# Performance work log

Hardware: AMD Instinct MI355X
Metric: run time of the kernel (lower is better)

Reference implementation:

```python
import jax, jax.numpy as jnp
import numpy as np

M = 512  # mem_dim

def silu(x):
    return x * jax.nn.sigmoid(x)

def layernorm(x, g, b, eps=1e-5):
    m = jnp.mean(x, axis=-1, keepdims=True)
    v = jnp.mean((x - m) ** 2, axis=-1, keepdims=True)
    return (x - m) * jax.lax.rsqrt(v + eps) * g + b

def dwconv(x, w, b):
    # x: [B,S,C], w: [C,1,K] depthwise, same padding
    y = jax.lax.conv_general_dilated(
        x.transpose(0, 2, 1), w, (1,), [(1, 1)],
        dimension_numbers=('NCH', 'OIH', 'NCH'), feature_group_count=x.shape[-1])
    return (y + b[None, :, None]).transpose(0, 2, 1)

def mlp(p, inp):
    W1, b1, W2, b2 = p
    return silu(inp @ W1.T + b1) @ W2.T + b2

def coeff(x, W1, b1, W2, b2):
    # x: [B,S,D] -> sigmoid scalar per token, averaged over batch -> [S]
    h = silu(jnp.einsum('bsd,hd->bsh', x, W1) + b1)
    c = jax.nn.sigmoid(jnp.einsum('bsh,oh->bso', h, W2) + b2)[..., 0]
    return jnp.mean(c, axis=0)

def setup_inputs() -> dict:
    key = jax.random.key(0)
    ks = jax.random.split(key, 24)
    B, S, D, H, CH, K = 8, 1024, 512, 32, 16, 3
    g = lambda k, shape, fan: jax.random.normal(k, shape, jnp.float32) / np.sqrt(fan)
    return {
        'x': jax.random.normal(ks[0], (B, S, D), jnp.float32),
        'Wk': g(ks[1], (M, D), D), 'Wv': g(ks[2], (M, D), D), 'Wq': g(ks[3], (M, D), D),
        'ck_w': g(ks[4], (M, 1, K), K), 'ck_b': g(ks[5], (M,), K),
        'cv_w': g(ks[6], (M, 1, K), K), 'cv_b': g(ks[7], (M,), K),
        'cq_w': g(ks[8], (M, 1, K), K), 'cq_b': g(ks[9], (M,), K),
        'ln_g': jnp.ones((M,), jnp.float32), 'ln_b': jnp.zeros((M,), jnp.float32),
        'W1': g(ks[10], (H, M), M), 'b1': jnp.zeros((H,), jnp.float32),
        'W2': g(ks[11], (M, H), H), 'b2': jnp.zeros((M,), jnp.float32),
        'aW1': g(ks[12], (CH, D), D), 'ab1': jnp.zeros((CH,), jnp.float32),
        'aW2': g(ks[13], (1, CH), CH), 'ab2': -2.0 * jnp.ones((1,), jnp.float32),
        'tW1': g(ks[14], (CH, D), D), 'tb1': jnp.zeros((CH,), jnp.float32),
        'tW2': g(ks[15], (1, CH), CH), 'tb2': -2.0 * jnp.ones((1,), jnp.float32),
        'eW1': g(ks[16], (CH, D), D), 'eb1': jnp.zeros((CH,), jnp.float32),
        'eW2': g(ks[17], (1, CH), CH), 'eb2': -2.0 * jnp.ones((1,), jnp.float32),
    }

def reference(x, Wk, Wv, Wq, ck_w, ck_b, cv_w, cv_b, cq_w, cq_b, ln_g, ln_b,
              W1, b1, W2, b2, aW1, ab1, aW2, ab2, tW1, tb1, tW2, tb2,
              eW1, eb1, eW2, eb2):
    k = layernorm(dwconv(x @ Wk.T, ck_w, ck_b), ln_g, ln_b)
    v = dwconv(x @ Wv.T, cv_w, cv_b)
    q = layernorm(dwconv(x @ Wq.T, cq_w, cq_b), ln_g, ln_b)
    alpha = coeff(x, aW1, ab1, aW2, ab2)  # [S]
    theta = coeff(x, tW1, tb1, tW2, tb2)
    eta = coeff(x, eW1, eb1, eW2, eb2)

    params0 = (W1, b1, W2, b2)
    S0 = jax.tree_util.tree_map(jnp.zeros_like, params0)

    def step(carry, xs_t):
        p, Sm = carry
        kt, vt, qt, a, th, e = xs_t  # kt/vt/qt: [B,M], a/th/e: scalar
        y = mlp(p, qt)  # output with pre-update params
        grad = jax.grad(lambda pp: jnp.mean((mlp(pp, kt) - vt) ** 2))(p)
        Sm = jax.tree_util.tree_map(lambda s, gi: e * s - th * gi, Sm, grad)
        p = jax.tree_util.tree_map(lambda pi, si: (1.0 - a) * pi + si, p, Sm)
        return (p, Sm), y

    xs = (k.transpose(1, 0, 2), v.transpose(1, 0, 2), q.transpose(1, 0, 2),
          alpha, theta, eta)
    _, ys = jax.lax.scan(step, (params0, S0), xs)
    return ys.transpose(1, 0, 2)  # [B,S,M]
```

## Files before the change

### kernel.cpp

```cpp
#include <hip/hip_runtime.h>
#include <hip/hip_bf16.h>
#include <cstdint>
#include <cstddef>

typedef __attribute__((ext_vector_type(8))) short bf16x8;
typedef __attribute__((ext_vector_type(4))) float f32x4;

#define DEV static __device__ __forceinline__

DEV float bf2f(uint16_t u){ union{uint32_t i; float f;} c; c.i = ((uint32_t)u) << 16; return c.f; }
DEV uint16_t f2bf(float f){ union{float f; uint32_t i;} c; c.f = f; uint32_t r = c.i + 0x7FFFu + ((c.i >> 16) & 1u); return (uint16_t)(r >> 16); }

DEV f32x4 mfma16(bf16x8 a, bf16x8 b, f32x4 c){
  return __builtin_amdgcn_mfma_f32_16x16x32_bf16(a, b, c, 0, 0, 0);
}

__global__ __launch_bounds__(128) void nltm_coeff(
    const float* __restrict__ x,
    const float* __restrict__ aW1, const float* __restrict__ ab1,
    const float* __restrict__ aW2, const float* __restrict__ ab2,
    const float* __restrict__ tW1, const float* __restrict__ tb1,
    const float* __restrict__ tW2, const float* __restrict__ tb2,
    const float* __restrict__ eW1, const float* __restrict__ eb1,
    const float* __restrict__ eW2, const float* __restrict__ eb2,
    float* __restrict__ gates)
{
  const int s = blockIdx.x, z = blockIdx.y;
  const int b = threadIdx.x >> 4, ch = threadIdx.x & 15;
  const float* w1 = (z==0)?aW1:(z==1)?tW1:eW1;
  const float* c1 = (z==0)?ab1:(z==1)?tb1:eb1;
  const float* w2 = (z==0)?aW2:(z==1)?tW2:eW2;
  const float* c2 = (z==0)?ab2:(z==1)?tb2:eb2;
  const float4* xp = (const float4*)(x + ((size_t)(b << 10) + s)*512);
  const float4* wp = (const float4*)(w1 + ch*512);
  float dot = 0.f;
  #pragma unroll 4
  for (int i = 0; i < 128; ++i){
    float4 a = xp[i], c = wp[i];
    dot += a.x*c.x + a.y*c.y + a.z*c.z + a.w*c.w;
  }
  dot += c1[ch];
  const float sg = 1.f / (1.f + __expf(-dot));
  float v = dot * sg * w2[ch];
  v += __shfl_xor(v, 1, 64);
  v += __shfl_xor(v, 2, 64);
  v += __shfl_xor(v, 4, 64);
  v += __shfl_xor(v, 8, 64);
  if (ch == 0){
    const float cc = 1.f / (1.f + __expf(-(v + c2[0])));
    atomicAdd(gates + (z << 10) + s, cc * 0.125f);
  }
}

__global__ __launch_bounds__(256) void nltm_gemm(
    const float* __restrict__ x, const float* __restrict__ Wk,
    const float* __restrict__ Wv, const float* __restrict__ Wq,
    uint16_t* __restrict__ preK, uint16_t* __restrict__ preV, uint16_t* __restrict__ preQ)
{
  __shared__ float As[16][132];
  __shared__ float Bs[16][132];
  const float* W = (blockIdx.z == 0) ? Wk : (blockIdx.z == 1) ? Wv : Wq;
  uint16_t* op  = (blockIdx.z == 0) ? preK : (blockIdx.z == 1) ? preV : preQ;
  const int tid = threadIdx.x;
  const int n0 = blockIdx.x << 7, m0 = blockIdx.y << 7;
  const int r = tid >> 1, cs = (tid & 1) << 3;
  const int ty = tid >> 4, tx = tid & 15;
  float acc[8][8];
  #pragma unroll
  for (int i = 0; i < 8; ++i)
    #pragma unroll
    for (int j = 0; j < 8; ++j) acc[i][j] = 0.f;

  for (int k0 = 0; k0 < 512; k0 += 16){
    float4 a0 = *(const float4*)(x + (size_t)(n0 + r)*512 + k0 + cs);
    float4 a1 = *(const float4*)(x + (size_t)(n0 + r)*512 + k0 + cs + 4);
    float4 b0 = *(const float4*)(W + (size_t)(m0 + r)*512 + k0 + cs);
    float4 b1 = *(const float4*)(W + (size_t)(m0 + r)*512 + k0 + cs + 4);
    __syncthreads();
    As[cs+0][r]=a0.x; As[cs+1][r]=a0.y; As[cs+2][r]=a0.z; As[cs+3][r]=a0.w;
    As[cs+4][r]=a1.x; As[cs+5][r]=a1.y; As[cs+6][r]=a1.z; As[cs+7][r]=a1.w;
    Bs[cs+0][r]=b0.x; Bs[cs+1][r]=b0.y; Bs[cs+2][r]=b0.z; Bs[cs+3][r]=b0.w;
    Bs[cs+4][r]=b1.x; Bs[cs+5][r]=b1.y; Bs[cs+6][r]=b1.z; Bs[cs+7][r]=b1.w;
    __syncthreads();
    #pragma unroll
    for (int kk = 0; kk < 16; ++kk){
      float4 av0 = *(const float4*)&As[kk][ty*8];
      float4 av1 = *(const float4*)&As[kk][ty*8+4];
      float4 bv0 = *(const float4*)&Bs[kk][tx*8];
      float4 bv1 = *(const float4*)&Bs[kk][tx*8+4];
      const float aa[8] = {av0.x,av0.y,av0.z,av0.w,av1.x,av1.y,av1.z,av1.w};
      const float bb[8] = {bv0.x,bv0.y,bv0.z,bv0.w,bv1.x,bv1.y,bv1.z,bv1.w};
      #pragma unroll
      for (int i = 0; i < 8; ++i)
        #pragma unroll
        for (int j = 0; j < 8; ++j)
          acc[i][j] = fmaf(aa[i], bb[j], acc[i][j]);
    }
  }
  #pragma unroll
  for (int i = 0; i < 8; ++i){
    const size_t n = (size_t)(n0 + ty*8 + i);
    uint4 v;
    v.x = (uint32_t)f2bf(acc[i][0]) | ((uint32_t)f2bf(acc[i][1]) << 16);
    v.y = (uint32_t)f2bf(acc[i][2]) | ((uint32_t)f2bf(acc[i][3]) << 16);
    v.z = (uint32_t)f2bf(acc[i][4]) | ((uint32_t)f2bf(acc[i][5]) << 16);
    v.w = (uint32_t)f2bf(acc[i][6]) | ((uint32_t)f2bf(acc[i][7]) << 16);
    *(uint4*)(op + n*512 + m0 + tx*8) = v;
  }
}

__global__ __launch_bounds__(512) void nltm_conv(
    const uint16_t* __restrict__ preK, const uint16_t* __restrict__ preV, const uint16_t* __restrict__ preQ,
    const float* __restrict__ ckw, const float* __restrict__ ckb,
    const float* __restrict__ cvw, const float* __restrict__ cvb,
    const float* __restrict__ cqw, const float* __restrict__ cqb,
    const float* __restrict__ lng, const float* __restrict__ lnb,
    uint16_t* __restrict__ postK, uint16_t* __restrict__ postV, uint16_t* __restrict__ postQ)
{
  const int z = blockIdx.y;
  const int b = blockIdx.x >> 10, s = blockIdx.x & 1023;
  const int m = threadIdx.x;
  const uint16_t* pre = (z==0)?preK:(z==1)?preV:preQ;
  const float* w  = (z==0)?ckw:(z==1)?cvw:cqw;
  const float* wb = (z==0)?ckb:(z==1)?cvb:cqb;
  uint16_t* post = (z==0)?postK:(z==1)?postV:postQ;
  const size_t base = ((size_t)(b << 10) + s)*512 + m;
  const float xm = (s > 0)    ? bf2f(pre[base - 512]) : 0.f;
  const float x0 = bf2f(pre[base]);
  const float xp = (s < 1023) ? bf2f(pre[base + 512]) : 0.f;
  float y = fmaf(w[m*3], xm, fmaf(w[m*3+1], x0, fmaf(w[m*3+2], xp, wb[m])));
  if (z != 1){
    __shared__ float red[2][8];
    float s1 = y, s2 = y*y;
    #pragma unroll
    for (int o = 32; o > 0; o >>= 1){
      s1 += __shfl_xor(s1, o, 64);
      s2 += __shfl_xor(s2, o, 64);
    }
    if ((threadIdx.x & 63) == 0){ red[0][threadIdx.x>>6] = s1; red[1][threadIdx.x>>6] = s2; }
    __syncthreads();
    float t1 = 0.f, t2 = 0.f;
    #pragma unroll
    for (int i = 0; i < 8; ++i){ t1 += red[0][i]; t2 += red[1][i]; }
    const float mean = t1 * (1.f/512.f);
    const float var  = t2 * (1.f/512.f) - mean*mean;
    y = (y - mean) * rsqrtf(var + 1e-5f) * lng[m] + lnb[m];
  }
  post[((size_t)(s << 3) + b)*512 + m] = f2bf(y);
}

__global__ __launch_bounds__(512, 2) void nltm_scan(
    const float* __restrict__ W1g, const float* __restrict__ b1g,
    const float* __restrict__ W2g, const float* __restrict__ b2g,
    const float* __restrict__ gates,
    const uint16_t* __restrict__ kq, const uint16_t* __restrict__ vq,
    const uint16_t* __restrict__ qq, float* __restrict__ out)
{
  constexpr uint32_t W1Lo=0, W2Lo=33280, W2To=66048, QLo=99328, KLo=107520,
                     VTo=115712, KTo=123904, GOTo=132096, HQSo=140288, HKSo=140928,
                     HKSTo=141568, GSITo=142080, GPTo=142592, SCRo=143104,
                     B1o=151296, B2o=151424;
  __shared__ __align__(16) char smem[153472];
  const int tid = threadIdx.x;
  const int lane = tid & 63;
  const int wid = tid >> 6;
  const int rb = lane & 15;
  const int kg = lane >> 4;

  float* b1L = (float*)(smem + B1o);
  float* b2L = (float*)(smem + B2o);

  float w1m[8][4], sm1[8][4], w2a[8][4], sma[8][4];
  #pragma unroll
  for (int i = 0; i < 8; ++i){
    const int tt = i >> 1, ht = i & 1;
    const int mA = (wid*4 + tt)*16;
    #pragma unroll
    for (int j = 0; j < 4; ++j){
      const int h1 = ht*16 + rb, m1 = mA + kg*4 + j;
      w1m[i][j] = W1g[h1*512 + m1];  sm1[i][j] = 0.f;
      w2a[i][j] = W2g[m1*32 + h1];   sma[i][j] = 0.f;
    }
  }
  float b2m = b2g[tid], smb2 = 0.f;
  float b1m = (tid < 32) ? b1g[tid] : 0.f, smb1 = 0.f;

  for (int idx = tid; idx < 16384; idx += 512){
    const int h = idx >> 9, m = idx & 511;
    *(uint16_t*)(smem + W1Lo + h*1040 + m*2) = f2bf(W1g[idx]);
    const int m2 = idx >> 5, h2 = idx & 31;
    const float w2v = W2g[idx];
    *(uint16_t*)(smem + W2Lo + m2*64 + (((h2>>3)^(m2&3))<<4) + ((h2&7)<<1)) = f2bf(w2v);
    *(uint16_t*)(smem + W2To + h2*1040 + m2*2) = f2bf(w2v);
  }
  if (tid < 32) b1L[tid] = b1g[tid];
  b2L[tid] = b2g[tid];

  #pragma unroll
  for (int i = 0; i < 4; ++i){
    const int g = ((i & 1) << 9) + tid;
    const int b = g >> 7, m4 = (g & 127) << 2;
    const uint16_t* src = (i < 2) ? kq : qq;
    uint2 v = *(const uint2*)(src + b*512 + m4);
    *(uint2*)(smem + ((i<2)?KLo:QLo) + b*1024 + (((m4>>3)^(b&7))<<4) + ((m4&7)<<1)) = v;
  }
  {
    const uint16_t* kp = kq + tid;
    const uint16_t* vp = vq + tid;
    uint32_t a0=kp[0],a1=kp[512],a2=kp[1024],a3=kp[1536],a4=kp[2048],a5=kp[2560],a6=kp[3072],a7=kp[3584];
    uint4 kt4; kt4.x=a0|(a1<<16); kt4.y=a2|(a3<<16); kt4.z=a4|(a5<<16); kt4.w=a6|(a7<<16);
    *(uint4*)(smem + KTo + tid*16) = kt4;
    uint32_t c0=vp[0],c1=vp[512],c2=vp[1024],c3=vp[1536],c4=vp[2048],c5=vp[2560],c6=vp[3072],c7=vp[3584];
    uint4 vt4; vt4.x=c0|(c1<<16); vt4.y=c2|(c3<<16); vt4.z=c4|(c5<<16); vt4.w=c6|(c7<<16);
    *(uint4*)(smem + VTo + tid*16) = vt4;
  }
  __syncthreads();

  const f32x4 cz = {0.f, 0.f, 0.f, 0.f};
  const bf16x8 zf = {0,0,0,0,0,0,0,0};

  for (int t = 0; t < 1024; ++t){
    const int tn = (t < 1023) ? (t + 1) : 1023;
    uint2 pf[4];
    #pragma unroll
    for (int i = 0; i < 4; ++i){
      const int g = ((i & 1) << 9) + tid;
      const int b = g >> 7, m4 = (g & 127) << 2;
      const uint16_t* src = (i < 2) ? kq : qq;
      pf[i] = *(const uint2*)(src + (size_t)tn*4096 + b*512 + m4);
    }
    uint4 ktpf, vtpf;
    {
      const uint16_t* kp = kq + (size_t)tn*4096 + tid;
      const uint16_t* vp = vq + (size_t)tn*4096 + tid;
      uint32_t a0=kp[0],a1=kp[512],a2=kp[1024],a3=kp[1536],a4=kp[2048],a5=kp[2560],a6=kp[3072],a7=kp[3584];
      ktpf.x=a0|(a1<<16); ktpf.y=a2|(a3<<16); ktpf.z=a4|(a5<<16); ktpf.w=a6|(a7<<16);
      uint32_t c0=vp[0],c1=vp[512],c2=vp[1024],c3=vp[1536],c4=vp[2048],c5=vp[2560],c6=vp[3072],c7=vp[3584];
      vtpf.x=c0|(c1<<16); vtpf.y=c2|(c3<<16); vtpf.z=c4|(c5<<16); vtpf.w=c6|(c7<<16);
    }
    const float a_t = gates[t], th_t = gates[1024 + t], e_t = gates[2048 + t];
    const float oma = 1.f - a_t;

    if (wid < 4){
      const int mm = wid >> 1, ht = wid & 1;
      const uint32_t srcO = mm ? KLo : QLo;
      const uint32_t w1row = W1Lo + (uint32_t)(ht*16 + rb)*1040;
      f32x4 acc0 = cz, acc1 = cz;
      #pragma unroll
      for (int k0 = 0; k0 < 16; k0 += 2){
        const int ch0 = (k0 << 2) + kg, ch1 = ((k0+1) << 2) + kg;
        bf16x8 a0 = (rb < 8) ? *(const bf16x8*)(smem + srcO + rb*1024 + ((ch0 ^ (rb&7)) << 4)) : zf;
        bf16x8 b0 = *(const bf16x8*)(smem + w1row + ((k0*32 + kg*8) << 1));
        acc0 = mfma16(a0, b0, acc0);
        bf16x8 a1 = (rb < 8) ? *(const bf16x8*)(smem + srcO + rb*1024 + ((ch1 ^ (rb&7)) << 4)) : zf;
        bf16x8 b1 = *(const bf16x8*)(smem + w1row + (((k0+1)*32 + kg*8) << 1));
        acc1 = mfma16(a1, b1, acc1);
      }
      f32x4 acc = acc0 + acc1;
      const int hh = ht*16 + rb;
      const float b1v = b1L[hh];
      float hsv[4], sdv[4];
      #pragma unroll
      for (int j = 0; j < 4; ++j){
        const float z = acc[j] + b1v;
        const float sg = 1.f / (1.f + __expf(-z));
        hsv[j] = z * sg;
        sdv[j] = sg * (1.f + z * (1.f - sg));
      }
      if (kg < 2){
        if (mm == 0){
          #pragma unroll
          for (int j = 0; j < 4; ++j)
            *(uint16_t*)(smem + HQSo + (kg*4+j)*80 + hh*2) = f2bf(hsv[j]);
        } else {
          #pragma unroll
          for (int j = 0; j < 4; ++j)
            *(uint16_t*)(smem + HKSo + (kg*4+j)*80 + hh*2) = f2bf(hsv[j]);
          uint2 hv; hv.x = (uint32_t)f2bf(hsv[0]) | ((uint32_t)f2bf(hsv[1])<<16);
                    hv.y = (uint32_t)f2bf(hsv[2]) | ((uint32_t)f2bf(hsv[3])<<16);
          *(uint2*)(smem + HKSTo + hh*16 + kg*8) = hv;
          uint2 sv; sv.x = (uint32_t)f2bf(sdv[0]) | ((uint32_t)f2bf(sdv[1])<<16);
                    sv.y = (uint32_t)f2bf(sdv[2]) | ((uint32_t)f2bf(sdv[3])<<16);
          *(uint2*)(smem + GSITo + hh*16 + kg*8) = sv;
        }
      }
    }
    __syncthreads();

    {
      bf16x8 aq = (rb < 8) ? *(const bf16x8*)(smem + HQSo + rb*80 + kg*16) : zf;
      bf16x8 ak = (rb < 8) ? *(const bf16x8*)(smem + HKSo + rb*80 + kg*16) : zf;
      #pragma unroll
      for (int i = 0; i < 4; ++i){
        const int mcol = (((wid << 2) + i) << 4) + rb;
        bf16x8 bw = *(const bf16x8*)(smem + W2Lo + mcol*64 + ((kg ^ (mcol & 3)) << 4));
        f32x4 cy = mfma16(aq, bw, cz);
        f32x4 ck = mfma16(ak, bw, cz);
        const float b2v = b2L[mcol];
        if (kg < 2){
          uint2 vvp = *(const uint2*)(smem + VTo + mcol*16 + kg*8);
          const float vv0 = bf2f((uint16_t)vvp.x), vv1 = bf2f((uint16_t)(vvp.x>>16));
          const float vv2 = bf2f((uint16_t)vvp.y), vv3 = bf2f((uint16_t)(vvp.y>>16));
          float gvv[4];
          gvv[0] = (ck[0] + b2v - vv0) * (2.f/4096.f);
          gvv[1] = (ck[1] + b2v - vv1) * (2.f/4096.f);
          gvv[2] = (ck[2] + b2v - vv2) * (2.f/4096.f);
          gvv[3] = (ck[3] + b2v - vv3) * (2.f/4096.f);
          #pragma unroll
          for (int j = 0; j < 4; ++j){
            const int bb = kg*4 + j;
            out[(((size_t)bb << 10) + t)*512 + mcol] = cy[j] + b2v;
          }
          uint2 gp; gp.x = (uint32_t)f2bf(gvv[0]) | ((uint32_t)f2bf(gvv[1])<<16);
                    gp.y = (uint32_t)f2bf(gvv[2]) | ((uint32_t)f2bf(gvv[3])<<16);
          *(uint2*)(smem + GOTo + mcol*16 + kg*8) = gp;
          #pragma unroll
          for (int j = 0; j < 4; ++j){
            const int bb = kg*4 + j;
            *(uint16_t*)(smem + KLo + bb*1024 + (((mcol>>3) ^ (bb&7))<<4) + ((mcol&7)<<1)) = f2bf(gvv[j]);
          }
        }
      }
    }
    __syncthreads();

    {
      const int ht = wid & 1, ks = wid >> 1;
      const int hcol = ht*16 + rb;
      f32x4 a0 = cz, a1 = cz;
      #pragma unroll
      for (int kk = 0; kk < 4; ++kk){
        const int mc8 = ks*16 + kk*4 + kg;
        bf16x8 av = (rb < 8) ? *(const bf16x8*)(smem + KLo + rb*1024 + ((mc8 ^ (rb&7)) << 4)) : zf;
        bf16x8 bv = *(const bf16x8*)(smem + W2To + hcol*1040 + (mc8 << 4));
        if (kk & 1) a1 = mfma16(av, bv, a1); else a0 = mfma16(av, bv, a0);
      }
      f32x4 acc = a0 + a1;
      *(f32x4*)(smem + SCRo + (((ht*4 + ks)*64 + lane) << 4)) = acc;
    }
    __syncthreads();

    if (wid < 2 && kg < 2){
      const int ht = wid;
      f32x4 s = cz;
      #pragma unroll
      for (int ks = 0; ks < 4; ++ks){
        f32x4 p = *(const f32x4*)(smem + SCRo + (((ht*4 + ks)*64 + lane) << 4));
        s += p;
      }
      uint2 gs = *(const uint2*)(smem + GSITo + (ht*16 + rb)*16 + kg*8);
      const float g0 = s[0]*bf2f((uint16_t)gs.x), g1 = s[1]*bf2f((uint16_t)(gs.x>>16));
      const float g2 = s[2]*bf2f((uint16_t)gs.y), g3 = s[3]*bf2f((uint16_t)(gs.y>>16));
      uint2 w; w.x = (uint32_t)f2bf(g0) | ((uint32_t)f2bf(g1)<<16);
               w.y = (uint32_t)f2bf(g2) | ((uint32_t)f2bf(g3)<<16);
      *(uint2*)(smem + GPTo + (ht*16 + rb)*16 + kg*8) = w;
    }
    __syncthreads();

    {
      #pragma unroll
      for (int i = 0; i < 4; ++i){
        const int g = ((i & 1) << 9) + tid;
        const int b = g >> 7, m4 = (g & 127) << 2;
        *(uint2*)(smem + ((i<2)?KLo:QLo) + b*1024 + (((m4>>3)^(b&7))<<4) + ((m4&7)<<1)) = pf[i];
      }

      bf16x8 hkF[2], gpF[2];
      #pragma unroll
      for (int ht = 0; ht < 2; ++ht){
        const int r0 = ht*16 + rb;
        hkF[ht] = (kg == 0) ? *(const bf16x8*)(smem + HKSTo + r0*16) : zf;
        gpF[ht] = (kg == 0) ? *(const bf16x8*)(smem + GPTo  + r0*16) : zf;
      }
      #pragma unroll
      for (int tt = 0; tt < 4; ++tt){
        const int mA = (wid*4 + tt)*16;
        const int r0 = mA + rb;
        bf16x8 ktf = (kg == 0) ? *(const bf16x8*)(smem + KTo  + r0*16) : zf;
        bf16x8 gof = (kg == 0) ? *(const bf16x8*)(smem + GOTo + r0*16) : zf;
        #pragma unroll
        for (int ht = 0; ht < 2; ++ht){
          const int i = tt*2 + ht;
          f32x4 g1 = mfma16(ktf, gpF[ht], cz);
          f32x4 g2 = mfma16(gof, hkF[ht], cz);
          float f1[4], f2[4];
          #pragma unroll
          for (int j = 0; j < 4; ++j){
            sm1[i][j] = e_t*sm1[i][j] - th_t*g1[j];
            w1m[i][j] = oma*w1m[i][j] + sm1[i][j];
            f1[j] = w1m[i][j];
            sma[i][j] = e_t*sma[i][j] - th_t*g2[j];
            w2a[i][j] = oma*w2a[i][j] + sma[i][j];
            f2[j] = w2a[i][j];
          }
          uint2 u1; u1.x = (uint32_t)f2bf(f1[0]) | ((uint32_t)f2bf(f1[1])<<16);
                    u1.y = (uint32_t)f2bf(f1[2]) | ((uint32_t)f2bf(f1[3])<<16);
          *(uint2*)(smem + W1Lo + (ht*16 + rb)*1040 + (mA + kg*4)*2) = u1;
          uint2 u2; u2.x = (uint32_t)f2bf(f2[0]) | ((uint32_t)f2bf(f2[1])<<16);
                    u2.y = (uint32_t)f2bf(f2[2]) | ((uint32_t)f2bf(f2[3])<<16);
          *(uint2*)(smem + W2To + (ht*16 + rb)*1040 + (mA + kg*4)*2) = u2;
        }
      }
      #pragma unroll
      for (int tt = 0; tt < 4; ++tt){
        const int m2 = (wid*4 + tt)*16 + rb;
        #pragma unroll
        for (int ht = 0; ht < 2; ++ht){
          const uint32_t cb = W2To + (uint32_t)m2*2 + (uint32_t)(ht*16 + kg*4)*1040;
          uint16_t t0 = *(const uint16_t*)(smem + cb);
          uint16_t t1 = *(const uint16_t*)(smem + cb + 1040);
          uint16_t t2 = *(const uint16_t*)(smem + cb + 2080);
          uint16_t t3 = *(const uint16_t*)(smem + cb + 3120);
          uint2 u; u.x = (uint32_t)t0 | ((uint32_t)t1<<16);
                   u.y = (uint32_t)t2 | ((uint32_t)t3<<16);
          *(uint2*)(smem + W2Lo + m2*64 + ((((ht<<1)+(kg>>1)) ^ (m2&3))<<4) + ((kg&1)<<3)) = u;
        }
      }
      {
        uint4 gv = *(const uint4*)(smem + GOTo + tid*16);
        float gb2 = bf2f((uint16_t)gv.x) + bf2f((uint16_t)(gv.x>>16))
                  + bf2f((uint16_t)gv.y) + bf2f((uint16_t)(gv.y>>16))
                  + bf2f((uint16_t)gv.z) + bf2f((uint16_t)(gv.z>>16))
                  + bf2f((uint16_t)gv.w) + bf2f((uint16_t)(gv.w>>16));
        smb2 = e_t*smb2 - th_t*gb2;
        b2m = oma*b2m + smb2;
        b2L[tid] = b2m;
      }
      if (tid < 32){
        uint4 gv = *(const uint4*)(smem + GPTo + tid*16);
        float gb1 = bf2f((uint16_t)gv.x) + bf2f((uint16_t)(gv.x>>16))
                  + bf2f((uint16_t)gv.y) + bf2f((uint16_t)(gv.y>>16))
                  + bf2f((uint16_t)gv.z) + bf2f((uint16_t)(gv.z>>16))
                  + bf2f((uint16_t)gv.w) + bf2f((uint16_t)(gv.w>>16));
        smb1 = e_t*smb1 - th_t*gb1;
        b1m = oma*b1m + smb1;
        b1L[tid] = b1m;
      }
      *(uint4*)(smem + KTo + tid*16) = ktpf;
      *(uint4*)(smem + VTo + tid*16) = vtpf;
    }
    __syncthreads();
  }
}

extern "C" void kernel_launch(void* const* d_in, const int* in_sizes, int n_in,
                              void* d_out, int out_size, void* d_ws, size_t ws_size,
                              hipStream_t stream)
{
  const float* x   = (const float*)d_in[0];
  const float* Wk  = (const float*)d_in[1];
  const float* Wv  = (const float*)d_in[2];
  const float* Wq  = (const float*)d_in[3];
  const float* ckw = (const float*)d_in[4];
  const float* ckb = (const float*)d_in[5];
  const float* cvw = (const float*)d_in[6];
  const float* cvb = (const float*)d_in[7];
  const float* cqw = (const float*)d_in[8];
  const float* cqb = (const float*)d_in[9];
  const float* lng = (const float*)d_in[10];
  const float* lnb = (const float*)d_in[11];
  const float* W1g = (const float*)d_in[12];
  const float* b1g = (const float*)d_in[13];
  const float* W2g = (const float*)d_in[14];
  const float* b2g = (const float*)d_in[15];
  const float* aW1 = (const float*)d_in[16];
  const float* ab1 = (const float*)d_in[17];
  const float* aW2 = (const float*)d_in[18];
  const float* ab2 = (const float*)d_in[19];
  const float* tW1 = (const float*)d_in[20];
  const float* tb1 = (const float*)d_in[21];
  const float* tW2 = (const float*)d_in[22];
  const float* tb2 = (const float*)d_in[23];
  const float* eW1 = (const float*)d_in[24];
  const float* eb1 = (const float*)d_in[25];
  const float* eW2 = (const float*)d_in[26];
  const float* eb2 = (const float*)d_in[27];

  char* ws = (char*)d_ws;
  float* gates = (float*)ws;
  uint16_t* preK  = (uint16_t*)(ws + 16384);
  uint16_t* preV  = preK + 4194304;
  uint16_t* preQ  = preV + 4194304;
  uint16_t* postK = preQ + 4194304;
  uint16_t* postV = postK + 4194304;
  uint16_t* postQ = postV + 4194304;

  hipMemsetAsync(gates, 0, 3*1024*sizeof(float), stream);
  nltm_coeff<<<dim3(1024,3), 128, 0, stream>>>(x, aW1,ab1,aW2,ab2, tW1,tb1,tW2,tb2,
                                               eW1,eb1,eW2,eb2, gates);
  nltm_gemm<<<dim3(64,4,3), 256, 0, stream>>>(x, Wk, Wv, Wq, preK, preV, preQ);
  nltm_conv<<<dim3(8192,3), 512, 0, stream>>>(preK,preV,preQ, ckw,ckb,cvw,cvb,cqw,cqb,
                                              lng,lnb, postK,postV,postQ);
  nltm_scan<<<dim3(1), dim3(512), 0, stream>>>(W1g, b1g, W2g, b2g, gates,
                                               postK, postV, postQ, (float*)d_out);
}
```

Before: 11.01 ms.

## Widen serial scan block to 1024 threads and pre-transpose K/V in conv

The single-block recurrent scan now runs with 1024 threads instead of 512. The first-layer MLP GEMM is split across all 16 waves with an LDS reduction, and Q and K hidden activations are stacked into one 16-row MFMA tile. The conv kernel is split into three launches and writes token-major transposed copies of K and V, so the scan loads them with vector reads instead of gathered 16-bit loads. Manual float-to-bf16 packing is replaced by v_cvt_pk_bf16_f32. In exchange, each step has an extra barrier, there is more scratch traffic through LDS, and fewer registers per thread remain under the 1024-thread launch bound.

```diff
diff --git a/kernel.cpp b/kernel.cpp
--- a/kernel.cpp
+++ b/kernel.cpp
@@ -10,6 +10,11 @@
 
 DEV float bf2f(uint16_t u){ union{uint32_t i; float f;} c; c.i = ((uint32_t)u) << 16; return c.f; }
 DEV uint16_t f2bf(float f){ union{float f; uint32_t i;} c; c.f = f; uint32_t r = c.i + 0x7FFFu + ((c.i >> 16) & 1u); return (uint16_t)(r >> 16); }
+DEV uint32_t cvtpk(float lo, float hi){
+  uint32_t r;
+  asm("v_cvt_pk_bf16_f32 %0, %1, %2" : "=v"(r) : "v"(lo), "v"(hi));
+  return r;
+}
 
 DEV f32x4 mfma16(bf16x8 a, bf16x8 b, f32x4 c){
   return __builtin_amdgcn_mfma_f32_16x16x32_bf16(a, b, c, 0, 0, 0);
@@ -110,26 +115,19 @@
 }
 
 __global__ __launch_bounds__(512) void nltm_conv(
-    const uint16_t* __restrict__ preK, const uint16_t* __restrict__ preV, const uint16_t* __restrict__ preQ,
-    const float* __restrict__ ckw, const float* __restrict__ ckb,
-    const float* __restrict__ cvw, const float* __restrict__ cvb,
-    const float* __restrict__ cqw, const float* __restrict__ cqb,
-    const float* __restrict__ lng, const float* __restrict__ lnb,
-    uint16_t* __restrict__ postK, uint16_t* __restrict__ postV, uint16_t* __restrict__ postQ)
+    const uint16_t* __restrict__ pre,
+    const float* __restrict__ w, const float* __restrict__ wb,
+    const float* __restrict__ lng, const float* __restrict__ lnb, const int doLN,
+    uint16_t* __restrict__ post, uint16_t* __restrict__ postT)
 {
-  const int z = blockIdx.y;
   const int b = blockIdx.x >> 10, s = blockIdx.x & 1023;
   const int m = threadIdx.x;
-  const uint16_t* pre = (z==0)?preK:(z==1)?preV:preQ;
-  const float* w  = (z==0)?ckw:(z==1)?cvw:cqw;
-  const float* wb = (z==0)?ckb:(z==1)?cvb:cqb;
-  uint16_t* post = (z==0)?postK:(z==1)?postV:postQ;
   const size_t base = ((size_t)(b << 10) + s)*512 + m;
   const float xm = (s > 0)    ? bf2f(pre[base - 512]) : 0.f;
   const float x0 = bf2f(pre[base]);
   const float xp = (s < 1023) ? bf2f(pre[base + 512]) : 0.f;
   float y = fmaf(w[m*3], xm, fmaf(w[m*3+1], x0, fmaf(w[m*3+2], xp, wb[m])));
-  if (z != 1){
+  if (doLN){
     __shared__ float red[2][8];
     float s1 = y, s2 = y*y;
     #pragma unroll
@@ -146,21 +144,23 @@
     const float var  = t2 * (1.f/512.f) - mean*mean;
     y = (y - mean) * rsqrtf(var + 1e-5f) * lng[m] + lnb[m];
   }
-  post[((size_t)(s << 3) + b)*512 + m] = f2bf(y);
-}
-
-__global__ __launch_bounds__(512, 2) void nltm_scan(
+  const uint16_t yb = f2bf(y);
+  if (post)  post[((size_t)(s << 3) + b)*512 + m] = yb;
+  if (postT) postT[(((size_t)s << 9) + m)*8 + b] = yb;
+}
+
+__global__ __launch_bounds__(1024) void nltm_scan(
     const float* __restrict__ W1g, const float* __restrict__ b1g,
     const float* __restrict__ W2g, const float* __restrict__ b2g,
     const float* __restrict__ gates,
-    const uint16_t* __restrict__ kq, const uint16_t* __restrict__ vq,
-    const uint16_t* __restrict__ qq, float* __restrict__ out)
+    const uint16_t* __restrict__ kN, const uint16_t* __restrict__ qN,
+    const uint16_t* __restrict__ kT, const uint16_t* __restrict__ vT,
+    float* __restrict__ out)
 {
-  constexpr uint32_t W1Lo=0, W2Lo=33280, W2To=66048, QLo=99328, KLo=107520,
-                     VTo=115712, KTo=123904, GOTo=132096, HQSo=140288, HKSo=140928,
-                     HKSTo=141568, GSITo=142080, GPTo=142592, SCRo=143104,
-                     B1o=151296, B2o=151424;
-  __shared__ __align__(16) char smem[153472];
+  constexpr uint32_t W1Lo=0, W2No=33280, W2To=66048, QKLo=99328, VTo=115712,
+                     KTo=123904, GOTo=132096, HQKo=140288, HKSTo=141312,
+                     SILPo=141824, GPTo=143872, SCRo=144384, B1o=160768, B2o=160896;
+  __shared__ __align__(16) char smem[162944];
   const int tid = threadIdx.x;
   const int lane = tid & 63;
   const int wid = tid >> 6;
@@ -170,11 +170,11 @@
   float* b1L = (float*)(smem + B1o);
   float* b2L = (float*)(smem + B2o);
 
-  float w1m[8][4], sm1[8][4], w2a[8][4], sma[8][4];
+  float w1m[4][4], sm1[4][4], w2a[4][4], sma[4][4];
   #pragma unroll
-  for (int i = 0; i < 8; ++i){
+  for (int i = 0; i < 4; ++i){
     const int tt = i >> 1, ht = i & 1;
-    const int mA = (wid*4 + tt)*16;
+    const int mA = (wid*2 + tt)*16;
     #pragma unroll
     for (int j = 0; j < 4; ++j){
       const int h1 = ht*16 + rb, m1 = mA + kg*4 + j;
@@ -182,142 +182,112 @@
       w2a[i][j] = W2g[m1*32 + h1];   sma[i][j] = 0.f;
     }
   }
-  float b2m = b2g[tid], smb2 = 0.f;
+  float b2m = (tid < 512) ? b2g[tid] : 0.f, smb2 = 0.f;
   float b1m = (tid < 32) ? b1g[tid] : 0.f, smb1 = 0.f;
 
-  for (int idx = tid; idx < 16384; idx += 512){
+  for (int idx = tid; idx < 16384; idx += 1024){
     const int h = idx >> 9, m = idx & 511;
     *(uint16_t*)(smem + W1Lo + h*1040 + m*2) = f2bf(W1g[idx]);
     const int m2 = idx >> 5, h2 = idx & 31;
     const float w2v = W2g[idx];
-    *(uint16_t*)(smem + W2Lo + m2*64 + (((h2>>3)^(m2&3))<<4) + ((h2&7)<<1)) = f2bf(w2v);
+    *(uint16_t*)(smem + W2No + m2*64 + (((h2>>3)^(m2&3))<<4) + ((h2&7)<<1)) = f2bf(w2v);
     *(uint16_t*)(smem + W2To + h2*1040 + m2*2) = f2bf(w2v);
   }
   if (tid < 32) b1L[tid] = b1g[tid];
-  b2L[tid] = b2g[tid];
-
-  #pragma unroll
-  for (int i = 0; i < 4; ++i){
-    const int g = ((i & 1) << 9) + tid;
-    const int b = g >> 7, m4 = (g & 127) << 2;
-    const uint16_t* src = (i < 2) ? kq : qq;
-    uint2 v = *(const uint2*)(src + b*512 + m4);
-    *(uint2*)(smem + ((i<2)?KLo:QLo) + b*1024 + (((m4>>3)^(b&7))<<4) + ((m4&7)<<1)) = v;
-  }
+  if (tid < 512) b2L[tid] = b2g[tid];
+
   {
-    const uint16_t* kp = kq + tid;
-    const uint16_t* vp = vq + tid;
-    uint32_t a0=kp[0],a1=kp[512],a2=kp[1024],a3=kp[1536],a4=kp[2048],a5=kp[2560],a6=kp[3072],a7=kp[3584];
-    uint4 kt4; kt4.x=a0|(a1<<16); kt4.y=a2|(a3<<16); kt4.z=a4|(a5<<16); kt4.w=a6|(a7<<16);
-    *(uint4*)(smem + KTo + tid*16) = kt4;
-    uint32_t c0=vp[0],c1=vp[512],c2=vp[1024],c3=vp[1536],c4=vp[2048],c5=vp[2560],c6=vp[3072],c7=vp[3584];
-    uint4 vt4; vt4.x=c0|(c1<<16); vt4.y=c2|(c3<<16); vt4.z=c4|(c5<<16); vt4.w=c6|(c7<<16);
-    *(uint4*)(smem + VTo + tid*16) = vt4;
+    const int b = tid >> 7, m4 = (tid & 127) << 2;
+    const uint32_t swz = (((m4>>3) ^ (b&7))<<4) + ((m4&7)<<1);
+    *(uint2*)(smem + QKLo + b*1024 + swz)       = *(const uint2*)(qN + tid*4);
+    *(uint2*)(smem + QKLo + (8+b)*1024 + swz)   = *(const uint2*)(kN + tid*4);
+    if (tid < 512) *(uint4*)(smem + KTo + tid*16) = *(const uint4*)(kT + tid*8);
+    else           *(uint4*)(smem + VTo + (tid-512)*16) = *(const uint4*)(vT + (tid-512)*8);
   }
   __syncthreads();
 
   const f32x4 cz = {0.f, 0.f, 0.f, 0.f};
   const bf16x8 zf = {0,0,0,0,0,0,0,0};
+  const int ht_ = wid & 1, ks_ = wid >> 1;
 
   for (int t = 0; t < 1024; ++t){
     const int tn = (t < 1023) ? (t + 1) : 1023;
-    uint2 pf[4];
-    #pragma unroll
-    for (int i = 0; i < 4; ++i){
-      const int g = ((i & 1) << 9) + tid;
-      const int b = g >> 7, m4 = (g & 127) << 2;
-      const uint16_t* src = (i < 2) ? kq : qq;
-      pf[i] = *(const uint2*)(src + (size_t)tn*4096 + b*512 + m4);
-    }
-    uint4 ktpf, vtpf;
-    {
-      const uint16_t* kp = kq + (size_t)tn*4096 + tid;
-      const uint16_t* vp = vq + (size_t)tn*4096 + tid;
-      uint32_t a0=kp[0],a1=kp[512],a2=kp[1024],a3=kp[1536],a4=kp[2048],a5=kp[2560],a6=kp[3072],a7=kp[3584];
-      ktpf.x=a0|(a1<<16); ktpf.y=a2|(a3<<16); ktpf.z=a4|(a5<<16); ktpf.w=a6|(a7<<16);
-      uint32_t c0=vp[0],c1=vp[512],c2=vp[1024],c3=vp[1536],c4=vp[2048],c5=vp[2560],c6=vp[3072],c7=vp[3584];
-      vtpf.x=c0|(c1<<16); vtpf.y=c2|(c3<<16); vtpf.z=c4|(c5<<16); vtpf.w=c6|(c7<<16);
-    }
+    uint2 pfq = *(const uint2*)(qN + (size_t)tn*4096 + tid*4);
+    uint2 pfk = *(const uint2*)(kN + (size_t)tn*4096 + tid*4);
+    uint4 pf4;
+    if (lane < 32) pf4 = *(const uint4*)(kT + (size_t)tn*4096 + (wid*32 + lane)*8);
+    else           pf4 = *(const uint4*)(vT + (size_t)tn*4096 + (wid*32 + lane - 32)*8);
     const float a_t = gates[t], th_t = gates[1024 + t], e_t = gates[2048 + t];
     const float oma = 1.f - a_t;
 
-    if (wid < 4){
-      const int mm = wid >> 1, ht = wid & 1;
-      const uint32_t srcO = mm ? KLo : QLo;
-      const uint32_t w1row = W1Lo + (uint32_t)(ht*16 + rb)*1040;
-      f32x4 acc0 = cz, acc1 = cz;
-      #pragma unroll
-      for (int k0 = 0; k0 < 16; k0 += 2){
-        const int ch0 = (k0 << 2) + kg, ch1 = ((k0+1) << 2) + kg;
-        bf16x8 a0 = (rb < 8) ? *(const bf16x8*)(smem + srcO + rb*1024 + ((ch0 ^ (rb&7)) << 4)) : zf;
-        bf16x8 b0 = *(const bf16x8*)(smem + w1row + ((k0*32 + kg*8) << 1));
-        acc0 = mfma16(a0, b0, acc0);
-        bf16x8 a1 = (rb < 8) ? *(const bf16x8*)(smem + srcO + rb*1024 + ((ch1 ^ (rb&7)) << 4)) : zf;
-        bf16x8 b1 = *(const bf16x8*)(smem + w1row + (((k0+1)*32 + kg*8) << 1));
-        acc1 = mfma16(a1, b1, acc1);
-      }
-      f32x4 acc = acc0 + acc1;
-      const int hh = ht*16 + rb;
-      const float b1v = b1L[hh];
-      float hsv[4], sdv[4];
+    {
+      const uint32_t w1row = W1Lo + (uint32_t)(ht_*16 + rb)*1040;
+      f32x4 acc = cz;
+      #pragma unroll
+      for (int u = 0; u < 2; ++u){
+        const int c32 = ks_*2 + u;
+        bf16x8 av = *(const bf16x8*)(smem + QKLo + rb*1024 + (((c32*4 + kg) ^ (rb&7)) << 4));
+        bf16x8 bv = *(const bf16x8*)(smem + w1row + c32*64 + kg*16);
+        acc = mfma16(av, bv, acc);
+      }
+      *(f32x4*)(smem + SCRo + ((wid*64 + lane) << 4)) = acc;
+    }
+    __syncthreads();
+
+    if (wid < 2){
+      const int ht = wid;
+      f32x4 s = cz;
+      #pragma unroll
+      for (int ks = 0; ks < 8; ++ks)
+        s += *(const f32x4*)(smem + SCRo + (((ks*2 + ht)*64 + lane) << 4));
+      const int h = ht*16 + rb;
+      const float b1v = b1L[h];
+      float hs[4], sd[4];
       #pragma unroll
       for (int j = 0; j < 4; ++j){
-        const float z = acc[j] + b1v;
+        const float z = s[j] + b1v;
         const float sg = 1.f / (1.f + __expf(-z));
-        hsv[j] = z * sg;
-        sdv[j] = sg * (1.f + z * (1.f - sg));
-      }
-      if (kg < 2){
-        if (mm == 0){
+        hs[j] = z * sg;
+        sd[j] = sg * (1.f + z * (1.f - sg));
+      }
+      #pragma unroll
+      for (int j = 0; j < 4; ++j)
+        *(uint16_t*)(smem + HQKo + (kg*4 + j)*64 + h*2) = f2bf(hs[j]);
+      if (kg >= 2){
+        uint2 hv; hv.x = cvtpk(hs[0], hs[1]); hv.y = cvtpk(hs[2], hs[3]);
+        *(uint2*)(smem + HKSTo + h*16 + (kg-2)*8) = hv;
+        f32x4 sv = {sd[0], sd[1], sd[2], sd[3]};
+        *(f32x4*)(smem + SILPo + h*64 + (kg-2)*16) = sv;
+      }
+    }
+    __syncthreads();
+
+    {
+      bf16x8 aF = *(const bf16x8*)(smem + HQKo + rb*64 + kg*16);
+      #pragma unroll
+      for (int u = 0; u < 2; ++u){
+        const int mcol = (wid*2 + u)*16 + rb;
+        bf16x8 bw = *(const bf16x8*)(smem + W2No + mcol*64 + ((kg ^ (mcol&3)) << 4));
+        f32x4 c = mfma16(aF, bw, cz);
+        const float b2v = b2L[mcol];
+        if (kg < 2){
           #pragma unroll
           for (int j = 0; j < 4; ++j)
-            *(uint16_t*)(smem + HQSo + (kg*4+j)*80 + hh*2) = f2bf(hsv[j]);
+            out[(((size_t)(kg*4 + j) << 10) + t)*512 + mcol] = c[j] + b2v;
         } else {
-          #pragma unroll
-          for (int j = 0; j < 4; ++j)
-            *(uint16_t*)(smem + HKSo + (kg*4+j)*80 + hh*2) = f2bf(hsv[j]);
-          uint2 hv; hv.x = (uint32_t)f2bf(hsv[0]) | ((uint32_t)f2bf(hsv[1])<<16);
-                    hv.y = (uint32_t)f2bf(hsv[2]) | ((uint32_t)f2bf(hsv[3])<<16);
-          *(uint2*)(smem + HKSTo + hh*16 + kg*8) = hv;
-          uint2 sv; sv.x = (uint32_t)f2bf(sdv[0]) | ((uint32_t)f2bf(sdv[1])<<16);
-                    sv.y = (uint32_t)f2bf(sdv[2]) | ((uint32_t)f2bf(sdv[3])<<16);
-          *(uint2*)(smem + GSITo + hh*16 + kg*8) = sv;
-        }
-      }
-    }
-    __syncthreads();
-
-    {
-      bf16x8 aq = (rb < 8) ? *(const bf16x8*)(smem + HQSo + rb*80 + kg*16) : zf;
-      bf16x8 ak = (rb < 8) ? *(const bf16x8*)(smem + HKSo + rb*80 + kg*16) : zf;
-      #pragma unroll
-      for (int i = 0; i < 4; ++i){
-        const int mcol = (((wid << 2) + i) << 4) + rb;
-        bf16x8 bw = *(const bf16x8*)(smem + W2Lo + mcol*64 + ((kg ^ (mcol & 3)) << 4));
-        f32x4 cy = mfma16(aq, bw, cz);
-        f32x4 ck = mfma16(ak, bw, cz);
-        const float b2v = b2L[mcol];
-        if (kg < 2){
-          uint2 vvp = *(const uint2*)(smem + VTo + mcol*16 + kg*8);
-          const float vv0 = bf2f((uint16_t)vvp.x), vv1 = bf2f((uint16_t)(vvp.x>>16));
-          const float vv2 = bf2f((uint16_t)vvp.y), vv3 = bf2f((uint16_t)(vvp.y>>16));
-          float gvv[4];
-          gvv[0] = (ck[0] + b2v - vv0) * (2.f/4096.f);
-          gvv[1] = (ck[1] + b2v - vv1) * (2.f/4096.f);
-          gvv[2] = (ck[2] + b2v - vv2) * (2.f/4096.f);
-          gvv[3] = (ck[3] + b2v - vv3) * (2.f/4096.f);
+          uint2 vt = *(const uint2*)(smem + VTo + mcol*16 + (kg-2)*8);
+          float g0 = (c[0] + b2v - bf2f((uint16_t)vt.x))       * 4.8828125e-4f;
+          float g1 = (c[1] + b2v - bf2f((uint16_t)(vt.x>>16))) * 4.8828125e-4f;
+          float g2 = (c[2] + b2v - bf2f((uint16_t)vt.y))       * 4.8828125e-4f;
+          float g3 = (c[3] + b2v - bf2f((uint16_t)(vt.y>>16))) * 4.8828125e-4f;
+          uint2 gp; gp.x = cvtpk(g0, g1); gp.y = cvtpk(g2, g3);
+          *(uint2*)(smem + GOTo + mcol*16 + (kg-2)*8) = gp;
           #pragma unroll
           for (int j = 0; j < 4; ++j){
-            const int bb = kg*4 + j;
-            out[(((size_t)bb << 10) + t)*512 + mcol] = cy[j] + b2v;
-          }
-          uint2 gp; gp.x = (uint32_t)f2bf(gvv[0]) | ((uint32_t)f2bf(gvv[1])<<16);
-                    gp.y = (uint32_t)f2bf(gvv[2]) | ((uint32_t)f2bf(gvv[3])<<16);
-          *(uint2*)(smem + GOTo + mcol*16 + kg*8) = gp;
-          #pragma unroll
-          for (int j = 0; j < 4; ++j){
-            const int bb = kg*4 + j;
-            *(uint16_t*)(smem + KLo + bb*1024 + (((mcol>>3) ^ (bb&7))<<4) + ((mcol&7)<<1)) = f2bf(gvv[j]);
+            const int b = kg*4 + j - 8;
+            const uint16_t gb = (uint16_t)((j & 1) ? ((j < 2 ? gp.x : gp.y) >> 16)
+                                                   : (j < 2 ? gp.x : gp.y));
+            *(uint16_t*)(smem + QKLo + (8+b)*1024 + (((mcol>>3) ^ (b&7)) << 4) + ((mcol&7) << 1)) = gb;
           }
         }
       }
@@ -325,18 +295,16 @@
     __syncthreads();
 
     {
-      const int ht = wid & 1, ks = wid >> 1;
-      const int hcol = ht*16 + rb;
-      f32x4 a0 = cz, a1 = cz;
-      #pragma unroll
-      for (int kk = 0; kk < 4; ++kk){
-        const int mc8 = ks*16 + kk*4 + kg;
-        bf16x8 av = (rb < 8) ? *(const bf16x8*)(smem + KLo + rb*1024 + ((mc8 ^ (rb&7)) << 4)) : zf;
-        bf16x8 bv = *(const bf16x8*)(smem + W2To + hcol*1040 + (mc8 << 4));
-        if (kk & 1) a1 = mfma16(av, bv, a1); else a0 = mfma16(av, bv, a0);
-      }
-      f32x4 acc = a0 + a1;
-      *(f32x4*)(smem + SCRo + (((ht*4 + ks)*64 + lane) << 4)) = acc;
+      const uint32_t w2row = W2To + (uint32_t)(ht_*16 + rb)*1040;
+      f32x4 acc = cz;
+      #pragma unroll
+      for (int u = 0; u < 2; ++u){
+        const int c32 = ks_*2 + u;
+        bf16x8 av = (rb < 8) ? *(const bf16x8*)(smem + QKLo + (8+rb)*1024 + (((c32*4 + kg) ^ (rb&7)) << 4)) : zf;
+        bf16x8 bv = *(const bf16x8*)(smem + w2row + c32*64 + kg*16);
+        acc = mfma16(av, bv, acc);
+      }
+      *(f32x4*)(smem + SCRo + ((wid*64 + lane) << 4)) = acc;
     }
     __syncthreads();
 
@@ -344,27 +312,16 @@
       const int ht = wid;
       f32x4 s = cz;
       #pragma unroll
-      for (int ks = 0; ks < 4; ++ks){
-        f32x4 p = *(const f32x4*)(smem + SCRo + (((ht*4 + ks)*64 + lane) << 4));
-        s += p;
-      }
-      uint2 gs = *(const uint2*)(smem + GSITo + (ht*16 + rb)*16 + kg*8);
-      const float g0 = s[0]*bf2f((uint16_t)gs.x), g1 = s[1]*bf2f((uint16_t)(gs.x>>16));
-      const float g2 = s[2]*bf2f((uint16_t)gs.y), g3 = s[3]*bf2f((uint16_t)(gs.y>>16));
-      uint2 w; w.x = (uint32_t)f2bf(g0) | ((uint32_t)f2bf(g1)<<16);
-               w.y = (uint32_t)f2bf(g2) | ((uint32_t)f2bf(g3)<<16);
-      *(uint2*)(smem + GPTo + (ht*16 + rb)*16 + kg*8) = w;
+      for (int ks = 0; ks < 8; ++ks)
+        s += *(const f32x4*)(smem + SCRo + (((ks*2 + ht)*64 + lane) << 4));
+      const int h = ht*16 + rb;
+      f32x4 sp = *(const f32x4*)(smem + SILPo + h*64 + kg*16);
+      uint2 w; w.x = cvtpk(s[0]*sp[0], s[1]*sp[1]); w.y = cvtpk(s[2]*sp[2], s[3]*sp[3]);
+      *(uint2*)(smem + GPTo + h*16 + kg*8) = w;
     }
     __syncthreads();
 
     {
-      #pragma unroll
-      for (int i = 0; i < 4; ++i){
-        const int g = ((i & 1) << 9) + tid;
-        const int b = g >> 7, m4 = (g & 127) << 2;
-        *(uint2*)(smem + ((i<2)?KLo:QLo) + b*1024 + (((m4>>3)^(b&7))<<4) + ((m4&7)<<1)) = pf[i];
-      }
-
       bf16x8 hkF[2], gpF[2];
       #pragma unroll
       for (int ht = 0; ht < 2; ++ht){
@@ -373,37 +330,31 @@
         gpF[ht] = (kg == 0) ? *(const bf16x8*)(smem + GPTo  + r0*16) : zf;
       }
       #pragma unroll
-      for (int tt = 0; tt < 4; ++tt){
-        const int mA = (wid*4 + tt)*16;
-        const int r0 = mA + rb;
-        bf16x8 ktf = (kg == 0) ? *(const bf16x8*)(smem + KTo  + r0*16) : zf;
-        bf16x8 gof = (kg == 0) ? *(const bf16x8*)(smem + GOTo + r0*16) : zf;
+      for (int tt = 0; tt < 2; ++tt){
+        const int mA = (wid*2 + tt)*16;
+        bf16x8 ktf = (kg == 0) ? *(const bf16x8*)(smem + KTo  + (mA + rb)*16) : zf;
+        bf16x8 gof = (kg == 0) ? *(const bf16x8*)(smem + GOTo + (mA + rb)*16) : zf;
         #pragma unroll
         for (int ht = 0; ht < 2; ++ht){
           const int i = tt*2 + ht;
           f32x4 g1 = mfma16(ktf, gpF[ht], cz);
           f32x4 g2 = mfma16(gof, hkF[ht], cz);
-          float f1[4], f2[4];
           #pragma unroll
           for (int j = 0; j < 4; ++j){
             sm1[i][j] = e_t*sm1[i][j] - th_t*g1[j];
             w1m[i][j] = oma*w1m[i][j] + sm1[i][j];
-            f1[j] = w1m[i][j];
             sma[i][j] = e_t*sma[i][j] - th_t*g2[j];
             w2a[i][j] = oma*w2a[i][j] + sma[i][j];
-            f2[j] = w2a[i][j];
           }
-          uint2 u1; u1.x = (uint32_t)f2bf(f1[0]) | ((uint32_t)f2bf(f1[1])<<16);
-                    u1.y = (uint32_t)f2bf(f1[2]) | ((uint32_t)f2bf(f1[3])<<16);
+          uint2 u1; u1.x = cvtpk(w1m[i][0], w1m[i][1]); u1.y = cvtpk(w1m[i][2], w1m[i][3]);
           *(uint2*)(smem + W1Lo + (ht*16 + rb)*1040 + (mA + kg*4)*2) = u1;
-          uint2 u2; u2.x = (uint32_t)f2bf(f2[0]) | ((uint32_t)f2bf(f2[1])<<16);
-                    u2.y = (uint32_t)f2bf(f2[2]) | ((uint32_t)f2bf(f2[3])<<16);
+          uint2 u2; u2.x = cvtpk(w2a[i][0], w2a[i][1]); u2.y = cvtpk(w2a[i][2], w2a[i][3]);
           *(uint2*)(smem + W2To + (ht*16 + rb)*1040 + (mA + kg*4)*2) = u2;
         }
       }
       #pragma unroll
-      for (int tt = 0; tt < 4; ++tt){
-        const int m2 = (wid*4 + tt)*16 + rb;
+      for (int tt = 0; tt < 2; ++tt){
+        const int m2 = (wid*2 + tt)*16 + rb;
         #pragma unroll
         for (int ht = 0; ht < 2; ++ht){
           const uint32_t cb = W2To + (uint32_t)m2*2 + (uint32_t)(ht*16 + kg*4)*1040;
@@ -411,12 +362,12 @@
           uint16_t t1 = *(const uint16_t*)(smem + cb + 1040);
           uint16_t t2 = *(const uint16_t*)(smem + cb + 2080);
           uint16_t t3 = *(const uint16_t*)(smem + cb + 3120);
-          uint2 u; u.x = (uint32_t)t0 | ((uint32_t)t1<<16);
-                   u.y = (uint32_t)t2 | ((uint32_t)t3<<16);
-          *(uint2*)(smem + W2Lo + m2*64 + ((((ht<<1)+(kg>>1)) ^ (m2&3))<<4) + ((kg&1)<<3)) = u;
+          uint2 u; u.x = (uint32_t)t0 | ((uint32_t)t1 << 16);
+                   u.y = (uint32_t)t2 | ((uint32_t)t3 << 16);
+          *(uint2*)(smem + W2No + m2*64 + ((((ht<<1)+(kg>>1)) ^ (m2&3)) << 4) + ((kg&1) << 3)) = u;
         }
       }
-      {
+      if (tid < 512){
         uint4 gv = *(const uint4*)(smem + GOTo + tid*16);
         float gb2 = bf2f((uint16_t)gv.x) + bf2f((uint16_t)(gv.x>>16))
                   + bf2f((uint16_t)gv.y) + bf2f((uint16_t)(gv.y>>16))
@@ -436,8 +387,14 @@
         b1m = oma*b1m + smb1;
         b1L[tid] = b1m;
       }
-      *(uint4*)(smem + KTo + tid*16) = ktpf;
-      *(uint4*)(smem + VTo + tid*16) = vtpf;
+      {
+        const int b = tid >> 7, m4 = (tid & 127) << 2;
+        const uint32_t swz = (((m4>>3) ^ (b&7))<<4) + ((m4&7)<<1);
+        *(uint2*)(smem + QKLo + b*1024 + swz)     = pfq;
+        *(uint2*)(smem + QKLo + (8+b)*1024 + swz) = pfk;
+        if (lane < 32) *(uint4*)(smem + KTo + (wid*32 + lane)*16)      = pf4;
+        else           *(uint4*)(smem + VTo + (wid*32 + lane - 32)*16) = pf4;
+      }
     }
     __syncthreads();
   }
@@ -478,19 +435,22 @@
 
   char* ws = (char*)d_ws;
   float* gates = (float*)ws;
-  uint16_t* preK  = (uint16_t*)(ws + 16384);
-  uint16_t* preV  = preK + 4194304;
-  uint16_t* preQ  = preV + 4194304;
-  uint16_t* postK = preQ + 4194304;
-  uint16_t* postV = postK + 4194304;
-  uint16_t* postQ = postV + 4194304;
+  uint16_t* preK   = (uint16_t*)(ws + 16384);
+  uint16_t* preV   = preK + 4194304;
+  uint16_t* preQ   = preV + 4194304;
+  uint16_t* postK  = preQ + 4194304;
+  uint16_t* postQ  = postK + 4194304;
+  uint16_t* postVT = postQ + 4194304;
+  uint16_t* postKT = preV;
 
   hipMemsetAsync(gates, 0, 3*1024*sizeof(float), stream);
   nltm_coeff<<<dim3(1024,3), 128, 0, stream>>>(x, aW1,ab1,aW2,ab2, tW1,tb1,tW2,tb2,
                                                eW1,eb1,eW2,eb2, gates);
   nltm_gemm<<<dim3(64,4,3), 256, 0, stream>>>(x, Wk, Wv, Wq, preK, preV, preQ);
-  nltm_conv<<<dim3(8192,3), 512, 0, stream>>>(preK,preV,preQ, ckw,ckb,cvw,cvb,cqw,cqb,
-                                              lng,lnb, postK,postV,postQ);
-  nltm_scan<<<dim3(1), dim3(512), 0, stream>>>(W1g, b1g, W2g, b2g, gates,
-                                               postK, postV, postQ, (float*)d_out);
-}
+  nltm_conv<<<dim3(8192), 512, 0, stream>>>(preV, cvw, cvb, lng, lnb, 0, nullptr, postVT);
+  nltm_conv<<<dim3(8192), 512, 0, stream>>>(preK, ckw, ckb, lng, lnb, 1, postK, postKT);
+  nltm_conv<<<dim3(8192), 512, 0, stream>>>(preQ, cqw, cqb, lng, lnb, 1, postQ, nullptr);
+  nltm_scan<<<dim3(1), dim3(1024), 0, stream>>>(W1g, b1g, W2g, b2g, gates,
+                                                postK, postQ, postKT, postVT,
+                                                (float*)d_out);
+}
```

Result: faster. 10.37 ms (-5.8%).
